# Kernel optimization log

Measured on AMD Instinct MI355X. Metric: run time of the kernel, lower is better.

## Reference

```python
import jax, jax.numpy as jnp
import numpy as np

EPS = 1e-5

def _ligru_layer(x, W, U, gamma, beta):
    # x: [B,T,F]; W: [2H,F]; U: [2H,H]; gamma/beta: [2H]
    B, T, _ = x.shape
    H = U.shape[1]
    w = jnp.einsum('btf,hf->bth', x, W)            # [B,T,2H] input projection
    # BatchNorm1d (training mode) over flattened (B*T, 2H)
    wf = w.reshape(B * T, 2 * H)
    mu = wf.mean(axis=0)
    var = wf.var(axis=0)
    wf = (wf - mu) / jnp.sqrt(var + EPS) * gamma + beta
    w = wf.reshape(B, T, 2 * H)

    Ut = U.T                                       # [H,2H]

    def step(h, wt):
        uh = h @ Ut                                # [B,2H]
        m = uh.mean(axis=-1, keepdims=True)
        v = uh.var(axis=-1, keepdims=True)
        uh = (uh - m) / jnp.sqrt(v + EPS)          # LayerNorm, no affine
        gates = wt + uh
        at, zt = gates[:, :H], gates[:, H:]
        zt = jax.nn.sigmoid(zt)
        h = zt * h + (1.0 - zt) * jax.nn.relu(at)
        return h, h

    h0 = jnp.zeros((B, H), x.dtype)
    _, hs = jax.lax.scan(step, h0, jnp.swapaxes(w, 0, 1))  # [T,B,H]
    return jnp.swapaxes(hs, 0, 1)                          # [B,T,H]


def setup_inputs() -> dict:
    key = jax.random.key(0)
    ks = jax.random.split(key, 5)
    B, T, F, H = 32, 1000, 80, 1024
    x = jax.random.normal(ks[0], (B, T, F), dtype=jnp.float32)
    W1 = jax.random.normal(ks[1], (2 * H, F), dtype=jnp.float32) * 0.05
    U1 = jax.random.normal(ks[2], (2 * H, H), dtype=jnp.float32) * 0.03
    W2 = jax.random.normal(ks[3], (2 * H, H), dtype=jnp.float32) * 0.03
    U2 = jax.random.normal(ks[4], (2 * H, H), dtype=jnp.float32) * 0.03
    g = jnp.ones((2 * H,), jnp.float32)
    b = jnp.zeros((2 * H,), jnp.float32)
    return {"x": x, "W1": W1, "U1": U1, "g1": g, "b1": b,
            "W2": W2, "U2": U2, "g2": g, "b2": b}


def reference(x, W1, U1, g1, b1, W2, U2, g2, b2):
    h = _ligru_layer(x, W1, U1, g1, b1)
    h = _ligru_layer(h, W2, U2, g2, b2)
    return h
```

## Files before the change

### kernel.cpp

```cpp
#include <hip/hip_runtime.h>

typedef unsigned short u16;
typedef _Float16 f16;
typedef f16 half8 __attribute__((ext_vector_type(8)));
typedef float float4v __attribute__((ext_vector_type(4)));

union HV { uint4 u; half8 h; u16 s[8]; };

__device__ __forceinline__ float h2f(u16 u) { union { u16 u; f16 h; } c; c.u = u; return (float)c.h; }
__device__ __forceinline__ u16 f2h(float f) { union { u16 u; f16 h; } c; c.h = (f16)f; return c.u; }

__device__ __forceinline__ void store_coh_u16(u16* p, unsigned v) {
  asm volatile("global_store_short %0, %1, off sc0 sc1" :: "v"(p), "v"(v) : "memory");
}
__device__ __forceinline__ void store_coh_u32(void* p, unsigned v) {
  asm volatile("global_store_dword %0, %1, off sc0 sc1" :: "v"(p), "v"(v) : "memory");
}
__device__ __forceinline__ void store_coh_f32x2(float* p, float a, float b) {
  unsigned long long pk = (unsigned long long)__float_as_uint(a) |
                          ((unsigned long long)__float_as_uint(b) << 32);
  asm volatile("global_store_dwordx2 %0, %1, off sc0 sc1" :: "v"(p), "v"(pk) : "memory");
}

__global__ void cvt_f32_f16(const float* __restrict__ s, u16* __restrict__ d, int n) {
  for (int i = blockIdx.x * blockDim.x + threadIdx.x; i < n; i += gridDim.x * blockDim.x)
    d[i] = f2h(s[i]);
}

__global__ __launch_bounds__(256) void gemm_f16(const u16* __restrict__ A, const u16* __restrict__ B,
                                                u16* __restrict__ C, int K) {
  __shared__ u16 As[128][40];
  __shared__ u16 Bs[128][40];
  const int tid = threadIdx.x, lane = tid & 63, wid = tid >> 6;
  const int col = lane & 15, quad = lane >> 4;
  const int wm = (wid & 1) * 64, wn = (wid >> 1) * 64;
  const int n0 = blockIdx.x * 128;
  const int m0 = blockIdx.y * 128;
  float4v acc[4][4];
  #pragma unroll
  for (int i = 0; i < 4; ++i)
    #pragma unroll
    for (int j = 0; j < 4; ++j) acc[i][j] = (float4v){0.f, 0.f, 0.f, 0.f};

  const int srow = tid >> 2;
  const int schunk = (tid & 3) * 8;

  for (int k0 = 0; k0 < K; k0 += 32) {
    __syncthreads();
    #pragma unroll
    for (int r2 = 0; r2 < 2; ++r2) {
      int row = srow + 64 * r2;
      int kk = k0 + schunk;
      uint4 av = {0, 0, 0, 0}, bv = {0, 0, 0, 0};
      if (kk + 8 <= K) {
        av = *(const uint4*)(A + (size_t)(m0 + row) * K + kk);
        bv = *(const uint4*)(B + (size_t)(n0 + row) * K + kk);
      }
      *(uint4*)&As[row][schunk] = av;
      *(uint4*)&Bs[row][schunk] = bv;
    }
    __syncthreads();
    HV af[4], bf[4];
    #pragma unroll
    for (int i = 0; i < 4; ++i) af[i].u = *(const uint4*)&As[wm + i * 16 + col][quad * 8];
    #pragma unroll
    for (int j = 0; j < 4; ++j) bf[j].u = *(const uint4*)&Bs[wn + j * 16 + col][quad * 8];
    #pragma unroll
    for (int i = 0; i < 4; ++i)
      #pragma unroll
      for (int j = 0; j < 4; ++j)
        acc[i][j] = __builtin_amdgcn_mfma_f32_16x16x32_f16(af[i].h, bf[j].h, acc[i][j], 0, 0, 0);
  }
  #pragma unroll
  for (int i = 0; i < 4; ++i)
    #pragma unroll
    for (int j = 0; j < 4; ++j)
      #pragma unroll
      for (int r = 0; r < 4; ++r) {
        int m = m0 + wm + i * 16 + quad * 4 + r;
        int n = n0 + wn + j * 16 + col;
        C[(size_t)m * 2048 + n] = f2h(acc[i][j][r]);
      }
}

__global__ void bn_stats(const u16* __restrict__ C, float* __restrict__ acc) {
  int c = blockIdx.x * 256 + threadIdx.x;
  int r0 = blockIdx.y * 256;
  float s = 0.f, q = 0.f;
  for (int r = r0; r < r0 + 256; ++r) {
    float v = h2f(C[(size_t)r * 2048 + c]);
    s += v; q += v * v;
  }
  atomicAdd(&acc[2 * c], s);
  atomicAdd(&acc[2 * c + 1], q);
}

__global__ void bn_final(const float* __restrict__ acc, const float* __restrict__ g,
                         const float* __restrict__ b, float2* __restrict__ ss) {
  int c = blockIdx.x * 256 + threadIdx.x;
  float mean = acc[2 * c] * (1.f / 32000.f);
  float var = acc[2 * c + 1] * (1.f / 32000.f) - mean * mean;
  float sc = g[c] * rsqrtf(var + 1e-5f);
  float2 o; o.x = sc; o.y = b[c] - mean * sc;
  ss[c] = o;
}

template <int OUT_F32>
__global__ __launch_bounds__(256, 1) void rec_kernel(
    const u16* __restrict__ w,
    const float2* __restrict__ ss,
    const u16* __restrict__ U,
    u16* hbuf,
    float* pstats,
    unsigned* flags,
    u16* out16, float* out32) {
  const int tid = threadIdx.x, lane = tid & 63, kh = tid >> 6;
  const int d = blockIdx.x >> 5, beta = blockIdx.x & 31;
  const int col = lane & 15, quad = lane >> 4;
  __shared__ float4v red[3][4][64];
  __shared__ unsigned rel2;
  if (tid == 0) rel2 = 0u;
  __syncthreads();

  const int ja = beta * 32 + col;

  HV ufA0[8], ufA1[8], ufZ0[8], ufZ1[8];
  #pragma unroll
  for (int kk = 0; kk < 8; ++kk) {
    int k = kh * 256 + kk * 32 + quad * 8;
    ufA0[kk].u = *(const uint4*)(U + (size_t)ja * 1024 + k);
    ufA1[kk].u = *(const uint4*)(U + (size_t)(ja + 16) * 1024 + k);
    ufZ0[kk].u = *(const uint4*)(U + (size_t)(1024 + ja) * 1024 + k);
    ufZ1[kk].u = *(const uint4*)(U + (size_t)(1024 + ja + 16) * 1024 + k);
  }
  float2 ssA0 = ss[ja], ssA1 = ss[ja + 16];
  float2 ssZ0 = ss[1024 + ja], ssZ1 = ss[1024 + ja + 16];

  u16* hb = hbuf + (size_t)d * 16 * 1024;
  float* ps = pstats + (size_t)d * 2048;
  unsigned* f1 = flags + (size_t)d * 512;
  unsigned* f2 = flags + 1024 + (size_t)d * 512;

  const u16* aptr = hb + (size_t)col * 1024 + kh * 256 + quad * 8;
  const int bloc = quad * 4;

  float hreg[4][2] = {{0.f, 0.f}, {0.f, 0.f}, {0.f, 0.f}, {0.f, 0.f}};
  u16 wa0[4], wa1[4], wz0[4], wz1[4];
  if (kh == 0) {
    #pragma unroll
    for (int r = 0; r < 4; ++r) {
      const u16* wr = w + ((size_t)(d * 16 + bloc + r) * 1000 + 0) * 2048 + ja;
      wa0[r] = wr[0]; wa1[r] = wr[16]; wz0[r] = wr[1024]; wz1[r] = wr[1040];
    }
  }

  for (int t = 0; t < 1000; ++t) {
    const unsigned tag = (unsigned)t + 1u;
    HV af[8];
    asm volatile(
        "global_load_dwordx4 %0, %8, off sc0 sc1\n\t"
        "global_load_dwordx4 %1, %8, off offset:64  sc0 sc1\n\t"
        "global_load_dwordx4 %2, %8, off offset:128 sc0 sc1\n\t"
        "global_load_dwordx4 %3, %8, off offset:192 sc0 sc1\n\t"
        "global_load_dwordx4 %4, %8, off offset:256 sc0 sc1\n\t"
        "global_load_dwordx4 %5, %8, off offset:320 sc0 sc1\n\t"
        "global_load_dwordx4 %6, %8, off offset:384 sc0 sc1\n\t"
        "global_load_dwordx4 %7, %8, off offset:448 sc0 sc1\n\t"
        "s_waitcnt vmcnt(0)"
        : "=v"(af[0].u), "=v"(af[1].u), "=v"(af[2].u), "=v"(af[3].u),
          "=v"(af[4].u), "=v"(af[5].u), "=v"(af[6].u), "=v"(af[7].u)
        : "v"(aptr)
        : "memory");

    float4v aA0 = (float4v){0.f, 0.f, 0.f, 0.f};
    float4v aA1 = (float4v){0.f, 0.f, 0.f, 0.f};
    float4v aZ0 = (float4v){0.f, 0.f, 0.f, 0.f};
    float4v aZ1 = (float4v){0.f, 0.f, 0.f, 0.f};
    #pragma unroll
    for (int kk = 0; kk < 8; ++kk) {
      aA0 = __builtin_amdgcn_mfma_f32_16x16x32_f16(af[kk].h, ufA0[kk].h, aA0, 0, 0, 0);
      aA1 = __builtin_amdgcn_mfma_f32_16x16x32_f16(af[kk].h, ufA1[kk].h, aA1, 0, 0, 0);
      aZ0 = __builtin_amdgcn_mfma_f32_16x16x32_f16(af[kk].h, ufZ0[kk].h, aZ0, 0, 0, 0);
      aZ1 = __builtin_amdgcn_mfma_f32_16x16x32_f16(af[kk].h, ufZ1[kk].h, aZ1, 0, 0, 0);
    }
    if (kh) {
      red[kh - 1][0][lane] = aA0; red[kh - 1][1][lane] = aA1;
      red[kh - 1][2][lane] = aZ0; red[kh - 1][3][lane] = aZ1;
    }
    __syncthreads();

    if (kh == 0) {
      aA0 += red[0][0][lane] + red[1][0][lane] + red[2][0][lane];
      aA1 += red[0][1][lane] + red[1][1][lane] + red[2][1][lane];
      aZ0 += red[0][2][lane] + red[1][2][lane] + red[2][2][lane];
      aZ1 += red[0][3][lane] + red[1][3][lane] + red[2][3][lane];
      const int p = t & 1;
      #pragma unroll
      for (int r = 0; r < 4; ++r) {
        float sv = aA0[r] + aA1[r] + aZ0[r] + aZ1[r];
        float qv = aA0[r] * aA0[r] + aA1[r] * aA1[r] + aZ0[r] * aZ0[r] + aZ1[r] * aZ1[r];
        #pragma unroll
        for (int off = 1; off < 16; off <<= 1) {
          sv += __shfl_xor(sv, off, 64);
          qv += __shfl_xor(qv, off, 64);
        }
        if (col == 0)
          store_coh_f32x2(ps + (((size_t)p * 16 + bloc + r) * 32 + beta) * 2, sv, qv);
      }
      asm volatile("s_waitcnt vmcnt(0)" ::: "memory");
      if (lane == 0) store_coh_u32(f1 + (size_t)beta * 16, tag);
      u16 wn_a0[4], wn_a1[4], wn_z0[4], wn_z1[4];
      {
        int tn = t < 999 ? t + 1 : t;
        #pragma unroll
        for (int r = 0; r < 4; ++r) {
          const u16* wr = w + ((size_t)(d * 16 + bloc + r) * 1000 + tn) * 2048 + ja;
          wn_a0[r] = wr[0]; wn_a1[r] = wr[16]; wn_z0[r] = wr[1024]; wn_z1[r] = wr[1040];
        }
      }
      {
        unsigned fv = tag; int ok;
        do {
          if (lane < 32)
            asm volatile("global_load_dword %0, %1, off sc0 sc1\n\ts_waitcnt vmcnt(0)"
                         : "=v"(fv) : "v"(f1 + (size_t)lane * 16) : "memory");
          ok = __all(lane < 32 ? (int)(fv >= tag) : 1);
        } while (!ok);
      }
      float4v cc[4];
      const float* rb = ps + ((size_t)p * 16 + bloc) * 64 + col * 4;
      asm volatile(
          "global_load_dwordx4 %0, %4, off sc0 sc1\n\t"
          "global_load_dwordx4 %1, %4, off offset:256 sc0 sc1\n\t"
          "global_load_dwordx4 %2, %4, off offset:512 sc0 sc1\n\t"
          "global_load_dwordx4 %3, %4, off offset:768 sc0 sc1\n\t"
          "s_waitcnt vmcnt(0)"
          : "=v"(cc[0]), "=v"(cc[1]), "=v"(cc[2]), "=v"(cc[3])
          : "v"(rb)
          : "memory");
      #pragma unroll
      for (int r = 0; r < 4; ++r) {
        float sm = cc[r][0] + cc[r][2];
        float sq = cc[r][1] + cc[r][3];
        #pragma unroll
        for (int off = 1; off < 16; off <<= 1) {
          sm += __shfl_xor(sm, off, 64);
          sq += __shfl_xor(sq, off, 64);
        }
        float mean = sm * (1.f / 2048.f);
        float var = sq * (1.f / 2048.f) - mean * mean;
        float inv = rsqrtf(var + 1e-5f);
        float ga0 = h2f(wa0[r]) * ssA0.x + ssA0.y + (aA0[r] - mean) * inv;
        float ga1 = h2f(wa1[r]) * ssA1.x + ssA1.y + (aA1[r] - mean) * inv;
        float gz0 = h2f(wz0[r]) * ssZ0.x + ssZ0.y + (aZ0[r] - mean) * inv;
        float gz1 = h2f(wz1[r]) * ssZ1.x + ssZ1.y + (aZ1[r] - mean) * inv;
        float z0 = 1.f / (1.f + __expf(-gz0));
        float z1 = 1.f / (1.f + __expf(-gz1));
        float h0 = z0 * hreg[r][0] + (1.f - z0) * (ga0 > 0.f ? ga0 : 0.f);
        float h1 = z1 * hreg[r][1] + (1.f - z1) * (ga1 > 0.f ? ga1 : 0.f);
        hreg[r][0] = h0; hreg[r][1] = h1;
        u16* hp = hb + (size_t)(bloc + r) * 1024 + ja;
        store_coh_u16(hp, (unsigned)f2h(h0));
        store_coh_u16(hp + 16, (unsigned)f2h(h1));
      }
      #pragma unroll
      for (int r = 0; r < 4; ++r) {
        wa0[r] = wn_a0[r]; wa1[r] = wn_a1[r];
        wz0[r] = wn_z0[r]; wz1[r] = wn_z1[r];
      }
      asm volatile("s_waitcnt vmcnt(0)" ::: "memory");
      if (lane == 0) store_coh_u32(f2 + (size_t)beta * 16, tag);
      #pragma unroll
      for (int r = 0; r < 4; ++r) {
        size_t orow = ((size_t)(d * 16 + bloc + r) * 1000 + t) * 1024 + ja;
        if (OUT_F32) { out32[orow] = hreg[r][0]; out32[orow + 16] = hreg[r][1]; }
        else         { out16[orow] = f2h(hreg[r][0]); out16[orow + 16] = f2h(hreg[r][1]); }
      }
      {
        unsigned fv = tag; int ok;
        do {
          if (lane < 32)
            asm volatile("global_load_dword %0, %1, off sc0 sc1\n\ts_waitcnt vmcnt(0)"
                         : "=v"(fv) : "v"(f2 + (size_t)lane * 16) : "memory");
          ok = __all(lane < 32 ? (int)(fv >= tag) : 1);
        } while (!ok);
      }
      if (tid == 0) *(volatile unsigned*)&rel2 = tag;
    } else {
      while (*(volatile unsigned*)&rel2 < tag) {}
    }
  }
}

extern "C" void kernel_launch(void* const* d_in, const int* in_sizes, int n_in,
                              void* d_out, int out_size, void* d_ws, size_t ws_size,
                              hipStream_t stream) {
  (void)in_sizes; (void)n_in; (void)out_size;
  const float* x  = (const float*)d_in[0];
  const float* W1 = (const float*)d_in[1];
  const float* U1 = (const float*)d_in[2];
  const float* g1 = (const float*)d_in[3];
  const float* b1 = (const float*)d_in[4];
  const float* W2 = (const float*)d_in[5];
  const float* U2 = (const float*)d_in[6];
  const float* g2 = (const float*)d_in[7];
  const float* b2 = (const float*)d_in[8];

  char* ws = (char*)d_ws;
  size_t o = 0;
  auto take = [&](size_t bytes) { size_t r = o; o = (o + bytes + 255) & ~(size_t)255; return r; };
  u16* wbuf  = (u16*)(ws + take(32000ULL * 2048 * 2));
  u16* h1seq = (u16*)(ws + take(32000ULL * 1024 * 2));
  u16* xb    = (u16*)(ws + take(32000ULL * 80 * 2));
  u16* W1b   = (u16*)(ws + take(2048ULL * 80 * 2));
  u16* W2b   = (u16*)(ws + take(2048ULL * 1024 * 2));
  u16* U1b   = (u16*)(ws + take(2048ULL * 1024 * 2));
  u16* U2b   = (u16*)(ws + take(2048ULL * 1024 * 2));
  float2* ss1 = (float2*)(ws + take(2048 * 8));
  float2* ss2 = (float2*)(ws + take(2048 * 8));
  size_t zbase = o;
  float* acc1 = (float*)(ws + take(2048 * 8));
  float* acc2 = (float*)(ws + take(2048 * 8));
  float* pstats1 = (float*)(ws + take(2ULL * 2 * 16 * 32 * 2 * 4));
  float* pstats2 = (float*)(ws + take(2ULL * 2 * 16 * 32 * 2 * 4));
  unsigned* flags1 = (unsigned*)(ws + take(2ULL * 2 * 32 * 16 * 4));
  unsigned* flags2 = (unsigned*)(ws + take(2ULL * 2 * 32 * 16 * 4));
  u16* hbuf1 = (u16*)(ws + take(32 * 1024 * 2));
  u16* hbuf2 = (u16*)(ws + take(32 * 1024 * 2));
  size_t zlen = o - zbase;
  if (ws_size < o) return;

  (void)hipMemsetAsync(ws + zbase, 0, zlen, stream);

  cvt_f32_f16<<<1280, 256, 0, stream>>>(x, xb, 32000 * 80);
  cvt_f32_f16<<<160, 256, 0, stream>>>(W1, W1b, 2048 * 80);
  cvt_f32_f16<<<1024, 256, 0, stream>>>(U1, U1b, 2048 * 1024);
  cvt_f32_f16<<<1024, 256, 0, stream>>>(W2, W2b, 2048 * 1024);
  cvt_f32_f16<<<1024, 256, 0, stream>>>(U2, U2b, 2048 * 1024);

  gemm_f16<<<dim3(16, 250), 256, 0, stream>>>(xb, W1b, wbuf, 80);
  bn_stats<<<dim3(8, 125), 256, 0, stream>>>(wbuf, acc1);
  bn_final<<<8, 256, 0, stream>>>(acc1, g1, b1, ss1);
  rec_kernel<0><<<64, 256, 0, stream>>>(wbuf, ss1, U1b, hbuf1, pstats1, flags1, h1seq, nullptr);

  gemm_f16<<<dim3(16, 250), 256, 0, stream>>>(h1seq, W2b, wbuf, 1024);
  bn_stats<<<dim3(8, 125), 256, 0, stream>>>(wbuf, acc2);
  bn_final<<<8, 256, 0, stream>>>(acc2, g2, b2, ss2);
  rec_kernel<1><<<64, 256, 0, stream>>>(wbuf, ss2, U2b, hbuf2, pstats2, flags2, nullptr, (float*)d_out);
}
```

Measured before the change: 13.73 ms.

## Embed step tags in partial-stat stores to drop the first flag barrier

Each partial sum and sum-of-squares is now stored together with the step tag in one 64-bit word. Readers poll the stats themselves until every tag matches, which removes the separate flag write, the wait before it, and the first cross-block flag spin. The shared-memory release flag is also dropped, so all four waves poll the global f2 flags directly instead of waves 1-3 spinning on LDS. In exchange, each poll reads twice as much data, and every wave now hits global memory while it waits.

```diff
diff --git a/kernel.cpp b/kernel.cpp
--- a/kernel.cpp
+++ b/kernel.cpp
@@ -16,9 +16,9 @@
 __device__ __forceinline__ void store_coh_u32(void* p, unsigned v) {
   asm volatile("global_store_dword %0, %1, off sc0 sc1" :: "v"(p), "v"(v) : "memory");
 }
-__device__ __forceinline__ void store_coh_f32x2(float* p, float a, float b) {
-  unsigned long long pk = (unsigned long long)__float_as_uint(a) |
-                          ((unsigned long long)__float_as_uint(b) << 32);
+__device__ __forceinline__ void store_coh_f32_tag(float* p, float val, unsigned tag) {
+  unsigned long long pk = (unsigned long long)__float_as_uint(val) |
+                          ((unsigned long long)tag << 32);
   asm volatile("global_store_dwordx2 %0, %1, off sc0 sc1" :: "v"(p), "v"(pk) : "memory");
 }
 
@@ -118,9 +118,6 @@
   const int d = blockIdx.x >> 5, beta = blockIdx.x & 31;
   const int col = lane & 15, quad = lane >> 4;
   __shared__ float4v red[3][4][64];
-  __shared__ unsigned rel2;
-  if (tid == 0) rel2 = 0u;
-  __syncthreads();
 
   const int ja = beta * 32 + col;
 
@@ -137,9 +134,8 @@
   float2 ssZ0 = ss[1024 + ja], ssZ1 = ss[1024 + ja + 16];
 
   u16* hb = hbuf + (size_t)d * 16 * 1024;
-  float* ps = pstats + (size_t)d * 2048;
-  unsigned* f1 = flags + (size_t)d * 512;
-  unsigned* f2 = flags + 1024 + (size_t)d * 512;
+  float* ps = pstats + (size_t)d * 4096;
+  unsigned* f2 = flags + (size_t)d * 512;
 
   const u16* aptr = hb + (size_t)col * 1024 + kh * 256 + quad * 8;
   const int bloc = quad * 4;
@@ -204,11 +200,12 @@
           sv += __shfl_xor(sv, off, 64);
           qv += __shfl_xor(qv, off, 64);
         }
-        if (col == 0)
-          store_coh_f32x2(ps + (((size_t)p * 16 + bloc + r) * 32 + beta) * 2, sv, qv);
-      }
-      asm volatile("s_waitcnt vmcnt(0)" ::: "memory");
-      if (lane == 0) store_coh_u32(f1 + (size_t)beta * 16, tag);
+        if (col == 0) {
+          float* dst = ps + (((size_t)p * 16 + bloc + r) * 32 + beta) * 4;
+          store_coh_f32_tag(dst, sv, tag);
+          store_coh_f32_tag(dst + 2, qv, tag);
+        }
+      }
       u16 wn_a0[4], wn_a1[4], wn_z0[4], wn_z1[4];
       {
         int tn = t < 999 ? t + 1 : t;
@@ -218,30 +215,35 @@
           wn_a0[r] = wr[0]; wn_a1[r] = wr[16]; wn_z0[r] = wr[1024]; wn_z1[r] = wr[1040];
         }
       }
-      {
-        unsigned fv = tag; int ok;
-        do {
-          if (lane < 32)
-            asm volatile("global_load_dword %0, %1, off sc0 sc1\n\ts_waitcnt vmcnt(0)"
-                         : "=v"(fv) : "v"(f1 + (size_t)lane * 16) : "memory");
-          ok = __all(lane < 32 ? (int)(fv >= tag) : 1);
-        } while (!ok);
-      }
-      float4v cc[4];
-      const float* rb = ps + ((size_t)p * 16 + bloc) * 64 + col * 4;
-      asm volatile(
-          "global_load_dwordx4 %0, %4, off sc0 sc1\n\t"
-          "global_load_dwordx4 %1, %4, off offset:256 sc0 sc1\n\t"
-          "global_load_dwordx4 %2, %4, off offset:512 sc0 sc1\n\t"
-          "global_load_dwordx4 %3, %4, off offset:768 sc0 sc1\n\t"
-          "s_waitcnt vmcnt(0)"
-          : "=v"(cc[0]), "=v"(cc[1]), "=v"(cc[2]), "=v"(cc[3])
-          : "v"(rb)
-          : "memory");
-      #pragma unroll
-      for (int r = 0; r < 4; ++r) {
-        float sm = cc[r][0] + cc[r][2];
-        float sq = cc[r][1] + cc[r][3];
+      float4v g[8];
+      const float* rb = ps + ((size_t)p * 16 + bloc) * 128 + col * 4;
+      int ok;
+      do {
+        asm volatile(
+            "global_load_dwordx4 %0, %8, off sc0 sc1\n\t"
+            "global_load_dwordx4 %1, %8, off offset:256  sc0 sc1\n\t"
+            "global_load_dwordx4 %2, %8, off offset:512  sc0 sc1\n\t"
+            "global_load_dwordx4 %3, %8, off offset:768  sc0 sc1\n\t"
+            "global_load_dwordx4 %4, %8, off offset:1024 sc0 sc1\n\t"
+            "global_load_dwordx4 %5, %8, off offset:1280 sc0 sc1\n\t"
+            "global_load_dwordx4 %6, %8, off offset:1536 sc0 sc1\n\t"
+            "global_load_dwordx4 %7, %8, off offset:1792 sc0 sc1\n\t"
+            "s_waitcnt vmcnt(0)"
+            : "=v"(g[0]), "=v"(g[1]), "=v"(g[2]), "=v"(g[3]),
+              "=v"(g[4]), "=v"(g[5]), "=v"(g[6]), "=v"(g[7])
+            : "v"(rb)
+            : "memory");
+        int okl = 1;
+        #pragma unroll
+        for (int i = 0; i < 8; ++i)
+          okl &= (__float_as_uint(g[i][1]) == tag && __float_as_uint(g[i][3]) == tag) ? 1 : 0;
+        ok = __all(okl);
+      } while (!ok);
+
+      #pragma unroll
+      for (int r = 0; r < 4; ++r) {
+        float sm = g[2 * r][0] + g[2 * r + 1][0];
+        float sq = g[2 * r][2] + g[2 * r + 1][2];
         #pragma unroll
         for (int off = 1; off < 16; off <<= 1) {
           sm += __shfl_xor(sm, off, 64);
@@ -276,18 +278,15 @@
         if (OUT_F32) { out32[orow] = hreg[r][0]; out32[orow + 16] = hreg[r][1]; }
         else         { out16[orow] = f2h(hreg[r][0]); out16[orow + 16] = f2h(hreg[r][1]); }
       }
-      {
-        unsigned fv = tag; int ok;
-        do {
-          if (lane < 32)
-            asm volatile("global_load_dword %0, %1, off sc0 sc1\n\ts_waitcnt vmcnt(0)"
-                         : "=v"(fv) : "v"(f2 + (size_t)lane * 16) : "memory");
-          ok = __all(lane < 32 ? (int)(fv >= tag) : 1);
-        } while (!ok);
-      }
-      if (tid == 0) *(volatile unsigned*)&rel2 = tag;
-    } else {
-      while (*(volatile unsigned*)&rel2 < tag) {}
+    }
+    {
+      unsigned fv = tag; int ok;
+      do {
+        if (lane < 32)
+          asm volatile("global_load_dword %0, %1, off sc0 sc1\n\ts_waitcnt vmcnt(0)"
+                       : "=v"(fv) : "v"(f2 + (size_t)lane * 16) : "memory");
+        ok = __all(lane < 32 ? (int)(fv >= tag) : 1);
+      } while (!ok);
     }
   }
 }
@@ -321,10 +320,10 @@
   size_t zbase = o;
   float* acc1 = (float*)(ws + take(2048 * 8));
   float* acc2 = (float*)(ws + take(2048 * 8));
-  float* pstats1 = (float*)(ws + take(2ULL * 2 * 16 * 32 * 2 * 4));
-  float* pstats2 = (float*)(ws + take(2ULL * 2 * 16 * 32 * 2 * 4));
-  unsigned* flags1 = (unsigned*)(ws + take(2ULL * 2 * 32 * 16 * 4));
-  unsigned* flags2 = (unsigned*)(ws + take(2ULL * 2 * 32 * 16 * 4));
+  float* pstats1 = (float*)(ws + take(2ULL * 2 * 16 * 32 * 4 * 4));
+  float* pstats2 = (float*)(ws + take(2ULL * 2 * 16 * 32 * 4 * 4));
+  unsigned* flags1 = (unsigned*)(ws + take(2ULL * 32 * 16 * 4));
+  unsigned* flags2 = (unsigned*)(ws + take(2ULL * 32 * 16 * 4));
   u16* hbuf1 = (u16*)(ws + take(32 * 1024 * 2));
   u16* hbuf2 = (u16*)(ws + take(32 * 1024 * 2));
   size_t zlen = o - zbase;
```

New measurement: 12.95 ms. 5.7% less time.
